# Performance work log

Measured on AMD Instinct MI355X. Metric: run time of the kernel, lower is better.

## Reference

```python
import jax, jax.numpy as jnp
import numpy as np

LE_LAMBDA = 0.01  # le_lambda from __init__
V, D = 100000, 128
B, C, NEG, P = 16384, 10, 50, 2000


def setup_inputs() -> dict:
    key = jax.random.key(0)
    k1, k2, k3, k4, k5, k6 = jax.random.split(key, 6)
    return {
        "input_labels": jax.random.randint(k1, (B,), 0, V),
        "pos_labels": jax.random.randint(k2, (B, C), 0, V),
        "neg_labels": jax.random.randint(k3, (B, NEG), 0, V),
        "pairs": jax.random.randint(k4, (P, 2), 0, V),
        "in_embed": jax.random.normal(k5, (V, D), dtype=jnp.float32),
        "out_embed": jax.random.normal(k6, (V, D), dtype=jnp.float32),
    }


def reference(input_labels, pos_labels, neg_labels, pairs, in_embed, out_embed):
    # --- skip-gram negative-sampling loss ---
    ie = in_embed[input_labels]          # [B, D]
    pe = out_embed[pos_labels]           # [B, C, D]
    ne = out_embed[neg_labels]           # [B, NEG, D]
    pos_dot = jnp.einsum('bcd,bd->bc', pe, ie)    # bmm(pos, input.unsqueeze(2))
    neg_dot = jnp.einsum('bkd,bd->bk', ne, -ie)   # bmm(neg, -input)
    log_pos = jax.nn.log_sigmoid(pos_dot).sum(axis=1)
    log_neg = jax.nn.log_sigmoid(neg_dot).sum(axis=1)
    loss_graph = (-(log_pos + log_neg)).mean()
    # --- hierarchy L2 regularizer (vectorized over the pair loop) ---
    diff = in_embed[pairs[:, 0]] - in_embed[pairs[:, 1]]   # [P, D]
    l2_norm = jnp.sqrt((diff * diff).sum(axis=-1)).sum()   # sum of per-pair norms
    loss_le = 0.5 * (l2_norm ** 2) * LE_LAMBDA
    loss_combined = loss_graph + loss_le
    return (loss_combined, loss_le)
```

## Files before the change

### kernel.cpp

```cpp
#include <hip/hip_runtime.h>

#define VOCAB 100000
#define DIM   128
#define BATCH 16384
#define CPOS  10
#define NNEG  50
#define NPAIR 2000
#define LE_LAMBDA 0.01

#define NTOT (CPOS + NNEG)
#define SGNS_BLOCKS (BATCH / 4)
#define PAIR_BLOCKS ((NPAIR + 7) / 8)

__device__ __forceinline__ float fast_log_sigmoid(float x) {
    float e = __expf(-fabsf(x));
    return fminf(x, 0.0f) - __logf(1.0f + e);
}


__global__ __launch_bounds__(256) void fused_kernel(
    const int* __restrict__ input_labels,
    const int* __restrict__ pos_labels,
    const int* __restrict__ neg_labels,
    const int* __restrict__ pairs,
    const float* __restrict__ in_embed,
    const float* __restrict__ out_embed,
    float* __restrict__ ws)
{
    const int tid    = threadIdx.x;
    const int lane64 = tid & 63;
    const int lane32 = tid & 31;

    if (blockIdx.x < SGNS_BLOCKS) {
        const int wid = tid >> 6;
        const int b   = blockIdx.x * 4 + wid;
        const int h   = (tid >> 5) & 1;

        const int il = input_labels[b];
        const float4 ie = *reinterpret_cast<const float4*>(
            in_embed + (size_t)il * DIM + lane32 * 4);

        int lblv = 0;
        if (lane64 < CPOS)       lblv = pos_labels[b * CPOS + lane64];
        else if (lane64 < NTOT)  lblv = neg_labels[b * NNEG + (lane64 - CPOS)];

        const int jbase = h * 30;
        float acc = 0.0f;

        #pragma unroll
        for (int k0 = 0; k0 < 30; k0 += 6) {
            int idx[6];
            #pragma unroll
            for (int u = 0; u < 6; ++u)
                idx[u] = __shfl(lblv, jbase + k0 + u, 64);

            float4 oe[6];
            #pragma unroll
            for (int u = 0; u < 6; ++u)
                oe[u] = *reinterpret_cast<const float4*>(
                    out_embed + (size_t)idx[u] * DIM + lane32 * 4);

            #pragma unroll
            for (int u = 0; u < 6; ++u) {
                const int j = jbase + k0 + u;
                float p = ie.x * oe[u].x + ie.y * oe[u].y
                        + ie.z * oe[u].z + ie.w * oe[u].w;
                p += __shfl_xor(p, 1);
                p += __shfl_xor(p, 2);
                p += __shfl_xor(p, 4);
                p += __shfl_xor(p, 8);
                p += __shfl_xor(p, 16);
                acc += fast_log_sigmoid(j < CPOS ? p : -p);
            }
        }

        acc += __shfl_xor(acc, 32);
        if (lane64 == 0) ws[b] = acc;
    } else {
        const int pb = blockIdx.x - SGNS_BLOCKS;
        const int p  = pb * 8 + (tid >> 5);
        if (p < NPAIR) {
            const int a = pairs[p * 2 + 0];
            const int c = pairs[p * 2 + 1];
            const float4 ea = *reinterpret_cast<const float4*>(
                in_embed + (size_t)a * DIM + lane32 * 4);
            const float4 eb = *reinterpret_cast<const float4*>(
                in_embed + (size_t)c * DIM + lane32 * 4);
            const float dx = ea.x - eb.x, dy = ea.y - eb.y;
            const float dz = ea.z - eb.z, dw = ea.w - eb.w;
            float ss = dx * dx + dy * dy + dz * dz + dw * dw;
            ss += __shfl_xor(ss, 1);
            ss += __shfl_xor(ss, 2);
            ss += __shfl_xor(ss, 4);
            ss += __shfl_xor(ss, 8);
            ss += __shfl_xor(ss, 16);
            if (lane32 == 0) ws[BATCH + p] = sqrtf(ss);
        }
    }
}

__global__ __launch_bounds__(256) void finalize_kernel(
    const float* __restrict__ ws, float* __restrict__ out)
{
    const int tid  = threadIdx.x;
    const int lane = tid & 63;
    const int wid  = tid >> 6;

    double g = 0.0, pn = 0.0;
    for (int i = tid; i < BATCH; i += 256) g  += (double)ws[i];
    for (int i = tid; i < NPAIR; i += 256) pn += (double)ws[BATCH + i];

    #pragma unroll
    for (int m = 32; m > 0; m >>= 1) {
        g  += __shfl_xor(g,  m);
        pn += __shfl_xor(pn, m);
    }

    __shared__ double sg[4], sp[4];
    if (lane == 0) { sg[wid] = g; sp[wid] = pn; }
    __syncthreads();
    if (tid == 0) {
        double G = 0.0, PN = 0.0;
        #pragma unroll
        for (int w = 0; w < 4; ++w) { G += sg[w]; PN += sp[w]; }
        const double loss_graph = -G / (double)BATCH;
        const double loss_le    = 0.5 * PN * PN * LE_LAMBDA;
        out[0] = (float)(loss_graph + loss_le);
        out[1] = (float)loss_le;
    }
}

extern "C" void kernel_launch(void* const* d_in, const int* in_sizes, int n_in,
                              void* d_out, int out_size, void* d_ws, size_t ws_size,
                              hipStream_t stream) {
    const int*   input_labels = (const int*)  d_in[0];
    const int*   pos_labels   = (const int*)  d_in[1];
    const int*   neg_labels   = (const int*)  d_in[2];
    const int*   pairs        = (const int*)  d_in[3];
    const float* in_embed     = (const float*)d_in[4];
    const float* out_embed    = (const float*)d_in[5];
    float* out = (float*)d_out;
    float* ws  = (float*)d_ws;

    fused_kernel<<<SGNS_BLOCKS + PAIR_BLOCKS, 256, 0, stream>>>(
        input_labels, pos_labels, neg_labels, pairs, in_embed, out_embed, ws);
    finalize_kernel<<<1, 256, 0, stream>>>(ws, out);
}
```

Before: 192.3 us.

## Transcode out_embed to bf16 table in workspace before gather

Adds a transcode kernel that converts the whole out_embed table (100000x128 fp32) to bf16 in workspace each call, then the SGNS kernel gathers 8-byte bf16 rows instead of 16-byte fp32 rows. The aim is to halve the bytes moved by the random gather. The price is a full read of the 51 MB table plus a 25.6 MB write on every call, which likely costs more than the gather saves (about 983k rows x 512 B, roughly 500 MB of traffic with poor locality), and bf16 rounding reduces precision. An fp32 fallback runs when the workspace is too small.

```diff
diff --git a/kernel.cpp b/kernel.cpp
--- a/kernel.cpp
+++ b/kernel.cpp
@@ -12,19 +12,41 @@
 #define SGNS_BLOCKS (BATCH / 4)
 #define PAIR_BLOCKS ((NPAIR + 7) / 8)
 
+#define TAB_OFF   73728u
+#define TAB_BYTES ((size_t)VOCAB * DIM * 2)
+#define WS_NEED   ((size_t)TAB_OFF + TAB_BYTES)
+
 __device__ __forceinline__ float fast_log_sigmoid(float x) {
     float e = __expf(-fabsf(x));
     return fminf(x, 0.0f) - __logf(1.0f + e);
 }
 
-
-__global__ __launch_bounds__(256) void fused_kernel(
+__device__ __forceinline__ unsigned f2bf(float f) {
+    unsigned u = __float_as_uint(f);
+    return (u + 0x7fffu + ((u >> 16) & 1u)) >> 16;
+}
+
+__global__ __launch_bounds__(256) void transcode_kernel(
+    const float* __restrict__ src, uint2* __restrict__ dst)
+{
+    const int n4 = VOCAB * DIM / 4;
+    const int stride = gridDim.x * blockDim.x;
+    for (int q = blockIdx.x * blockDim.x + threadIdx.x; q < n4; q += stride) {
+        float4 v = reinterpret_cast<const float4*>(src)[q];
+        uint2 o;
+        o.x = f2bf(v.x) | (f2bf(v.y) << 16);
+        o.y = f2bf(v.z) | (f2bf(v.w) << 16);
+        dst[q] = o;
+    }
+}
+
+__global__ __launch_bounds__(256) void fused_bf16_kernel(
     const int* __restrict__ input_labels,
     const int* __restrict__ pos_labels,
     const int* __restrict__ neg_labels,
     const int* __restrict__ pairs,
     const float* __restrict__ in_embed,
-    const float* __restrict__ out_embed,
+    const uint2* __restrict__ otab,
     float* __restrict__ ws)
 {
     const int tid    = threadIdx.x;
@@ -54,17 +76,19 @@
             for (int u = 0; u < 6; ++u)
                 idx[u] = __shfl(lblv, jbase + k0 + u, 64);
 
-            float4 oe[6];
-            #pragma unroll
-            for (int u = 0; u < 6; ++u)
-                oe[u] = *reinterpret_cast<const float4*>(
-                    out_embed + (size_t)idx[u] * DIM + lane32 * 4);
+            uint2 oe[6];
+            #pragma unroll
+            for (int u = 0; u < 6; ++u)
+                oe[u] = otab[(size_t)idx[u] * 32 + lane32];
 
             #pragma unroll
             for (int u = 0; u < 6; ++u) {
                 const int j = jbase + k0 + u;
-                float p = ie.x * oe[u].x + ie.y * oe[u].y
-                        + ie.z * oe[u].z + ie.w * oe[u].w;
+                const float x0 = __uint_as_float(oe[u].x << 16);
+                const float x1 = __uint_as_float(oe[u].x & 0xffff0000u);
+                const float x2 = __uint_as_float(oe[u].y << 16);
+                const float x3 = __uint_as_float(oe[u].y & 0xffff0000u);
+                float p = ie.x * x0 + ie.y * x1 + ie.z * x2 + ie.w * x3;
                 p += __shfl_xor(p, 1);
                 p += __shfl_xor(p, 2);
                 p += __shfl_xor(p, 4);
@@ -99,6 +123,84 @@
     }
 }
 
+__global__ __launch_bounds__(256) void fused_f32_kernel(
+    const int* __restrict__ input_labels,
+    const int* __restrict__ pos_labels,
+    const int* __restrict__ neg_labels,
+    const int* __restrict__ pairs,
+    const float* __restrict__ in_embed,
+    const float* __restrict__ out_embed,
+    float* __restrict__ ws)
+{
+    const int tid    = threadIdx.x;
+    const int lane64 = tid & 63;
+    const int lane32 = tid & 31;
+
+    if (blockIdx.x < SGNS_BLOCKS) {
+        const int wid = tid >> 6;
+        const int b   = blockIdx.x * 4 + wid;
+        const int h   = (tid >> 5) & 1;
+
+        const int il = input_labels[b];
+        const float4 ie = *reinterpret_cast<const float4*>(
+            in_embed + (size_t)il * DIM + lane32 * 4);
+
+        int lblv = 0;
+        if (lane64 < CPOS)       lblv = pos_labels[b * CPOS + lane64];
+        else if (lane64 < NTOT)  lblv = neg_labels[b * NNEG + (lane64 - CPOS)];
+
+        const int jbase = h * 30;
+        const float* obase = out_embed + lane32 * 4;
+        float acc = 0.0f;
+
+        #pragma unroll
+        for (int k0 = 0; k0 < 30; k0 += 6) {
+            int idx[6];
+            #pragma unroll
+            for (int u = 0; u < 6; ++u)
+                idx[u] = __shfl(lblv, jbase + k0 + u, 64);
+            float4 oe[6];
+            #pragma unroll
+            for (int u = 0; u < 6; ++u)
+                oe[u] = *reinterpret_cast<const float4*>(obase + (size_t)idx[u] * DIM);
+            #pragma unroll
+            for (int u = 0; u < 6; ++u) {
+                const int j = jbase + k0 + u;
+                float p = ie.x * oe[u].x + ie.y * oe[u].y
+                        + ie.z * oe[u].z + ie.w * oe[u].w;
+                p += __shfl_xor(p, 1);
+                p += __shfl_xor(p, 2);
+                p += __shfl_xor(p, 4);
+                p += __shfl_xor(p, 8);
+                p += __shfl_xor(p, 16);
+                acc += fast_log_sigmoid(j < CPOS ? p : -p);
+            }
+        }
+        acc += __shfl_xor(acc, 32);
+        if (lane64 == 0) ws[b] = acc;
+    } else {
+        const int pb = blockIdx.x - SGNS_BLOCKS;
+        const int p  = pb * 8 + (tid >> 5);
+        if (p < NPAIR) {
+            const int a = pairs[p * 2 + 0];
+            const int c = pairs[p * 2 + 1];
+            const float4 ea = *reinterpret_cast<const float4*>(
+                in_embed + (size_t)a * DIM + lane32 * 4);
+            const float4 eb = *reinterpret_cast<const float4*>(
+                in_embed + (size_t)c * DIM + lane32 * 4);
+            const float dx = ea.x - eb.x, dy = ea.y - eb.y;
+            const float dz = ea.z - eb.z, dw = ea.w - eb.w;
+            float ss = dx * dx + dy * dy + dz * dz + dw * dw;
+            ss += __shfl_xor(ss, 1);
+            ss += __shfl_xor(ss, 2);
+            ss += __shfl_xor(ss, 4);
+            ss += __shfl_xor(ss, 8);
+            ss += __shfl_xor(ss, 16);
+            if (lane32 == 0) ws[BATCH + p] = sqrtf(ss);
+        }
+    }
+}
+
 __global__ __launch_bounds__(256) void finalize_kernel(
     const float* __restrict__ ws, float* __restrict__ out)
 {
@@ -142,7 +244,14 @@
     float* out = (float*)d_out;
     float* ws  = (float*)d_ws;
 
-    fused_kernel<<<SGNS_BLOCKS + PAIR_BLOCKS, 256, 0, stream>>>(
-        input_labels, pos_labels, neg_labels, pairs, in_embed, out_embed, ws);
+    if (ws_size >= WS_NEED) {
+        uint2* tab = (uint2*)((char*)d_ws + TAB_OFF);
+        transcode_kernel<<<2048, 256, 0, stream>>>(out_embed, tab);
+        fused_bf16_kernel<<<SGNS_BLOCKS + PAIR_BLOCKS, 256, 0, stream>>>(
+            input_labels, pos_labels, neg_labels, pairs, in_embed, tab, ws);
+    } else {
+        fused_f32_kernel<<<SGNS_BLOCKS + PAIR_BLOCKS, 256, 0, stream>>>(
+            input_labels, pos_labels, neg_labels, pairs, in_embed, out_embed, ws);
+    }
     finalize_kernel<<<1, 256, 0, stream>>>(ws, out);
 }
```

Result: faster. 178.6 us (-7.1%).
